# Kernel tuning notes

Hardware: AMD Instinct MI355X
Metric: run time of the kernel (lower is better)

## Reference

```python
import jax, jax.numpy as jnp
import numpy as np

B, IN, H = 4096, 1024, 1024
G = 5  # i, f, o, c_hat, s gates

def setup_inputs() -> dict:
    key = jax.random.key(0)
    ks = jax.random.split(key, 24)
    s_in = 1.0 / np.sqrt(IN)
    s_h = 1.0 / np.sqrt(H)
    s_cat = 1.0 / np.sqrt(IN + H)
    inp = {
        'x': jax.random.normal(ks[0], (B, IN), jnp.float32),
        'h_prev': jax.random.normal(ks[1], (B, H), jnp.float32),
        'c_prev': jax.random.normal(ks[2], (B, H), jnp.float32),
        'ssg_state': jax.random.normal(ks[3], (B, H), jnp.float32),
        # stacked gate weights, torch Linear convention y = x @ W.T + b
        'Wx': jax.random.uniform(ks[4], (G, H, IN), jnp.float32, -s_in, s_in),
        'bWx': jax.random.uniform(ks[5], (G, H), jnp.float32, -s_in, s_in),
        'Ux': jax.random.uniform(ks[6], (G, H, H), jnp.float32, -s_h, s_h),
        'bUx': jax.random.uniform(ks[7], (G, H), jnp.float32, -s_h, s_h),
        # alpha MLP: Linear(IN+H -> H), ReLU, Linear(H -> 1), Sigmoid
        'a1_w': jax.random.uniform(ks[8], (H, IN + H), jnp.float32, -s_cat, s_cat),
        'a1_b': jax.random.uniform(ks[9], (H,), jnp.float32, -s_cat, s_cat),
        'a2_w': jax.random.uniform(ks[10], (1, H), jnp.float32, -s_h, s_h),
        'a2_b': jax.random.uniform(ks[11], (1,), jnp.float32, -s_h, s_h),
        'r1_w': jax.random.uniform(ks[12], (H, H), jnp.float32, -s_h, s_h),
        'r1_b': jax.random.uniform(ks[13], (H,), jnp.float32, -s_h, s_h),
        'r2_w': jax.random.uniform(ks[14], (H, H), jnp.float32, -s_h, s_h),
        'r2_b': jax.random.uniform(ks[15], (H,), jnp.float32, -s_h, s_h),
        'r3_w': jax.random.uniform(ks[16], (H, H), jnp.float32, -s_h, s_h),
        'r3_b': jax.random.uniform(ks[17], (H,), jnp.float32, -s_h, s_h),
        'ssg_w': jax.random.uniform(ks[18], (H, H), jnp.float32, -s_h, s_h),
        'ssg_b': jax.random.uniform(ks[19], (H,), jnp.float32, -s_h, s_h),
    }
    return inp


def reference(x, h_prev, c_prev, ssg_state, Wx, bWx, Ux, bUx,
              a1_w, a1_b, a2_w, a2_b, r1_w, r1_b, r2_w, r2_b, r3_w, r3_b,
              ssg_w, ssg_b):
    # all 5 gate pre-activations in two batched GEMMs: [G, B, H]
    g = (jnp.einsum('bi,ghi->gbh', x, Wx) + bWx[:, None, :]
         + jnp.einsum('bh,gkh->gbk', h_prev, Ux) + bUx[:, None, :])
    i_t = jax.nn.sigmoid(g[0])
    f_t = jax.nn.sigmoid(g[1])
    o_t = jax.nn.sigmoid(g[2])
    c_hat_t = jnp.tanh(g[3])
    s_t = jax.nn.sigmoid(g[4])  # computed as in original (unused when ssg_state given)

    combined = jnp.concatenate([x, h_prev], axis=-1)  # [B, IN+H]
    a_hidden = jax.nn.relu(combined @ a1_w.T + a1_b)
    alpha_t = jax.nn.sigmoid(a_hidden @ a2_w.T + a2_b)  # [B, 1]

    ssg_new = (ssg_state + h_prev) @ ssg_w.T + ssg_b  # ssg_state is not None branch

    c_t = f_t * c_prev + i_t * c_hat_t * s_t * alpha_t * ssg_new

    r = jax.nn.relu(h_prev @ r1_w.T + r1_b)
    r = jax.nn.relu(r @ r2_w.T + r2_b)
    residual = r @ r3_w.T + r3_b

    c_t = c_t + residual
    h_t = o_t * jnp.tanh(c_t)
    return (h_t, c_t, ssg_new)
```

## Files before the change

### kernel.cpp

```cpp
#include <hip/hip_runtime.h>
#include <hip/hip_bf16.h>

#define B_DIM 4096
#define H_DIM 1024
#define K1    2048
#define N1    6144
#define N2    2048
#define NT1   (K1 / 64)

typedef __attribute__((ext_vector_type(8))) short bf16x8;
typedef __attribute__((ext_vector_type(4))) float f32x4;

__device__ __forceinline__ unsigned short f2bf(float f) {
  unsigned int x = __float_as_uint(f);
  x += 0x7fffu + ((x >> 16) & 1u);
  return (unsigned short)(x >> 16);
}
__device__ __forceinline__ float bf2f(unsigned short u) {
  return __uint_as_float(((unsigned int)u) << 16);
}
__device__ __forceinline__ float fast_sigmoid(float x) {
  return __builtin_amdgcn_rcpf(1.0f + __expf(-x));
}
__device__ __forceinline__ float fast_tanh(float x) {
  return 1.0f - 2.0f * __builtin_amdgcn_rcpf(1.0f + __expf(2.0f * x));
}
__device__ __forceinline__ void gload_lds16(const void* g, void* l) {
  __builtin_amdgcn_global_load_lds(
      (const __attribute__((address_space(1))) void*)g,
      (__attribute__((address_space(3))) void*)l, 16, 0, 0);
}

__device__ __forceinline__ int swz1k(int x) {
  return x ^ (((x >> 9) & 1) << 5);
}

__global__ __launch_bounds__(256) void prep_kernel(
    const float* __restrict__ x, const float* __restrict__ h,
    const float* __restrict__ ssg_state,
    const float* __restrict__ Wx, const float* __restrict__ Ux,
    const float* __restrict__ a1_w,
    const float* __restrict__ ssg_w, const float* __restrict__ r1_w,
    const float* __restrict__ r2_w, const float* __restrict__ r3_w,
    unsigned short* __restrict__ combined,
    unsigned short* __restrict__ ssg_in,
    unsigned short* __restrict__ hprev_bf,
    unsigned short* __restrict__ W1,
    unsigned short* __restrict__ W2,
    unsigned short* __restrict__ W3,
    unsigned short* __restrict__ W4)
{
  const size_t NV0 = (size_t)B_DIM * K1 / 4;
  const size_t NV1 = (size_t)B_DIM * H_DIM / 4;
  const size_t NV2 = NV1;
  const size_t NV3 = (size_t)N1 * K1 / 4;
  const size_t NV4 = (size_t)N2 * H_DIM / 4;
  const size_t NV5 = (size_t)H_DIM * H_DIM / 4;
  const size_t total = NV0 + NV1 + NV2 + NV3 + NV4 + NV5 + NV5;
  const size_t stride = (size_t)gridDim.x * blockDim.x;

  for (size_t v = (size_t)blockIdx.x * blockDim.x + threadIdx.x; v < total; v += stride) {
    size_t idx = v;
    const float* src;
    unsigned short* dst;
    if (idx < NV0) {
      size_t e = idx * 4, b = e >> 11, k = e & 2047;
      src = (k < 1024) ? &x[(b << 10) + k] : &h[(b << 10) + (k - 1024)];
      dst = &combined[e];
    } else if ((idx -= NV0) < NV1) {
      size_t e = idx * 4;
      float4 a = *(const float4*)&ssg_state[e];
      float4 c = *(const float4*)&h[e];
      ushort4 o;
      o.x = f2bf(a.x + c.x); o.y = f2bf(a.y + c.y);
      o.z = f2bf(a.z + c.z); o.w = f2bf(a.w + c.w);
      *(ushort4*)&ssg_in[e] = o;
      continue;
    } else if ((idx -= NV1) < NV2) {
      size_t e = idx * 4; src = &h[e]; dst = &hprev_bf[e];
    } else if ((idx -= NV2) < NV3) {
      size_t e = idx * 4, n = e >> 11, k = e & 2047;
      if (n < 5120) src = (k < 1024) ? &Wx[(n << 10) + k] : &Ux[(n << 10) + (k - 1024)];
      else          src = &a1_w[((n - 5120) << 11) + k];
      dst = &W1[e];
    } else if ((idx -= NV3) < NV4) {
      size_t e = idx * 4, n = e >> 10, k = e & 1023;
      src = (n < 1024) ? &ssg_w[(n << 10) + k] : &r1_w[((n - 1024) << 10) + k];
      dst = &W2[e];
    } else if ((idx -= NV4) < NV5) {
      size_t e = idx * 4; src = &r2_w[e]; dst = &W3[e];
    } else {
      idx -= NV5;
      size_t e = idx * 4; src = &r3_w[e]; dst = &W4[e];
    }
    float4 a = *(const float4*)src;
    ushort4 o;
    o.x = f2bf(a.x); o.y = f2bf(a.y); o.z = f2bf(a.z); o.w = f2bf(a.w);
    *(ushort4*)dst = o;
  }
}

__global__ __launch_bounds__(512, 2) void gemm8p_mode0(
    const unsigned short* __restrict__ A,
    const unsigned short* __restrict__ W,
    const float* __restrict__ bWx, const float* __restrict__ bUx,
    const float* __restrict__ a1_b,
    unsigned short* __restrict__ gates,
    unsigned short* __restrict__ a_hidden)
{
  __shared__ unsigned short lds[49152];

  const int tid  = threadIdx.x;
  const int wave = tid >> 6;
  const int lane = tid & 63;
  const int wm = wave >> 2;
  const int wn = wave & 3;

  const int NWG = (B_DIM / 128) * (N1 / 256);
  const int swz = (blockIdx.x & 7) * (NWG / 8) + (blockIdx.x >> 3);
  const int ntn = N1 / 256;
  const int tm = swz / ntn, tn = swz % ntn;
  const int tmB = tm * 128, tnB = tn * 256;

  const int sidx = swz1k(lane * 16);
  const int r_l  = sidx >> 6;
  const int kel  = (sidx & 63) >> 1;
  const unsigned short* pA[2];
  const unsigned short* pB[2];
#pragma unroll
  for (int j = 0; j < 2; ++j) {
    const int rr = wave * 16 + r_l;
    const int kk0 = j * 32 + kel;
    pA[j] = A + (size_t)(tmB + rr) * K1 + kk0;
    pB[j] = W + (size_t)(tnB + rr) * K1 + kk0;
  }

#define STAGE_A(tt) do { const int p_ = (tt) & 1;                                \
    gload_lds16(pA[0] + (size_t)(tt) * 64,                                       \
                &lds[p_ * 24576 + (wave * 2 + 0) * 512]);                        \
    gload_lds16(pA[1] + (size_t)(tt) * 64,                                       \
                &lds[p_ * 24576 + (wave * 2 + 1) * 512]); } while (0)
#define STAGE_B(tt, h_) do { const int p_ = (tt) & 1;                            \
    gload_lds16(pB[0] + (size_t)(h_) * 128 * K1 + (tt) * 64,                     \
                &lds[p_ * 24576 + 8192 + (h_) * 8192 + (wave * 2 + 0) * 512]);   \
    gload_lds16(pB[1] + (size_t)(h_) * 128 * K1 + (tt) * 64,                     \
                &lds[p_ * 24576 + 8192 + (h_) * 8192 + (wave * 2 + 1) * 512]); } while (0)

  const int loc = swz1k((lane & 15) * 64 + (lane >> 4) * 16);

  f32x4 acc[4][4];
#pragma unroll
  for (int m = 0; m < 4; ++m)
#pragma unroll
    for (int n = 0; n < 4; ++n) acc[m][n] = (f32x4){0.f, 0.f, 0.f, 0.f};

  STAGE_A(0); STAGE_B(0, 0); STAGE_B(0, 1);

#define MFMA16(aV, bV) do {                                                      \
    _Pragma("unroll")                                                            \
    for (int n = 0; n < 4; ++n) {                                                \
      _Pragma("unroll")                                                          \
      for (int m = 0; m < 4; ++m)                                                \
        acc[m][n] = __builtin_amdgcn_mfma_f32_16x16x32_bf16(                     \
            aV[m], bV[n], acc[m][n], 0, 0, 0);                                   \
    } } while (0)

  const char* lchar = (const char*)lds;
  for (int t = 0; t < NT1; ++t) {
    asm volatile("s_waitcnt vmcnt(0)" ::: "memory");
    __builtin_amdgcn_s_barrier();

    const char* base = lchar + (t & 1) * 49152;
    const char* bA = base + wm * 8192 + loc;
    const char* bB = base + 16384 + wn * 8192 + loc;

    bf16x8 a0[4], a1[4], b0[4], b1[4];
#pragma unroll
    for (int n = 0; n < 4; ++n) b0[n] = *(const bf16x8*)(bB + (2 * n + 0) * 1024);
#pragma unroll
    for (int m = 0; m < 4; ++m) a0[m] = *(const bf16x8*)(bA + (2 * m + 0) * 1024);
    if (t + 1 < NT1) STAGE_A(t + 1);
#pragma unroll
    for (int n = 0; n < 4; ++n) b1[n] = *(const bf16x8*)(bB + (2 * n + 1) * 1024);
#pragma unroll
    for (int m = 0; m < 4; ++m) a1[m] = *(const bf16x8*)(bA + (2 * m + 1) * 1024);
    if (t + 1 < NT1) { STAGE_B(t + 1, 0); STAGE_B(t + 1, 1); }

    __builtin_amdgcn_s_setprio(1);
    MFMA16(a0, b0);
    __builtin_amdgcn_s_setprio(0);
    __builtin_amdgcn_s_setprio(1);
    MFMA16(a1, b1);
    __builtin_amdgcn_s_setprio(0);
  }
#undef MFMA16
#undef STAGE_A
#undef STAGE_B

  unsigned short* slab = &lds[wave * 1024];
  const int l15 = lane & 15, lq4 = (lane >> 4) << 2;
  const int lr8 = lane >> 3, lc8 = lane & 7;
  const bool isgate = (tn < 20);
  const int g = tn >> 2;
  const int colg0 = (isgate ? (tn & 3) : (tn - 20)) * 256 + wn * 64;
  unsigned short* outbase = isgate ? (gates + (size_t)g * ((size_t)B_DIM * 1024))
                                   : a_hidden;
  const int rowg0 = tmB + wm * 64;
  float biasv[4];
#pragma unroll
  for (int fn = 0; fn < 4; ++fn) {
    const int c = colg0 + fn * 16 + l15;
    biasv[fn] = isgate ? (bWx[g * 1024 + c] + bUx[g * 1024 + c]) : a1_b[c];
  }
  __builtin_amdgcn_s_barrier();
#pragma unroll
  for (int fm = 0; fm < 4; ++fm) {
#pragma unroll
    for (int fn = 0; fn < 4; ++fn) {
      f32x4 v = acc[fm][fn];
#pragma unroll
      for (int j = 0; j < 4; ++j) {
        const int row = lq4 + j;
        const float xv = v[j] + biasv[fn];
        const float res = isgate ? ((g == 3) ? fast_tanh(xv) : fast_sigmoid(xv))
                                 : fmaxf(xv, 0.f);
        const int colb = ((fn * 16 + l15) * 2) ^ (((row >> 2) & 3) << 5);
        slab[(row * 128 + colb) >> 1] = f2bf(res);
      }
    }
    asm volatile("s_waitcnt lgkmcnt(0)" ::: "memory");
    __builtin_amdgcn_sched_barrier(0);
#pragma unroll
    for (int rd = 0; rd < 2; ++rd) {
      const int row = rd * 8 + lr8;
      const int cb = (lc8 * 16) ^ (((row >> 2) & 3) << 5);
      bf16x8 pk = *(const bf16x8*)((const char*)slab + row * 128 + cb);
      const size_t r = (size_t)(rowg0 + fm * 16 + row);
      *(bf16x8*)&outbase[r * 1024 + colg0 + lc8 * 8] = pk;
    }
    asm volatile("s_waitcnt lgkmcnt(0)" ::: "memory");
    __builtin_amdgcn_sched_barrier(0);
  }
}

template <int MODE>
__global__ __launch_bounds__(256, 3) void gemm_bf16(
    const unsigned short* __restrict__ A0g,
    const unsigned short* __restrict__ A1g,
    const unsigned short* __restrict__ Wg,
    const int M, const int N, const int K,
    const float* __restrict__ b0, const float* __restrict__ b1,
    void* __restrict__ out0, void* __restrict__ out1)
{
  __shared__ unsigned short As[128 * 64];
  __shared__ unsigned short Bs[128 * 64];

  const int tid  = threadIdx.x;
  const int wave = tid >> 6;
  const int lane = tid & 63;
  const int wm = wave >> 1, wn = wave & 1;

  const int ntn = N >> 7;
  const int tm = blockIdx.x / ntn;
  const int tn = blockIdx.x % ntn;

  const unsigned short* Ag = A0g;
  if (MODE == 1 && tn >= 8) Ag = A1g;

  const int lrow = lane >> 3;
  const int lk   = (lane & 7) * 8;
  size_t a_off[4], b_off[4];
#pragma unroll
  for (int i = 0; i < 4; ++i) {
    int c = wave * 4 + i;
    int row = c * 8 + lrow;
    a_off[i] = (size_t)(tm * 128 + row) * K + lk;
    b_off[i] = (size_t)(tn * 128 + row) * K + lk;
  }

  f32x4 acc[4][4];
#pragma unroll
  for (int m = 0; m < 4; ++m)
#pragma unroll
    for (int n = 0; n < 4; ++n) acc[m][n] = (f32x4){0.f, 0.f, 0.f, 0.f};

  const int arow  = wm * 64 + (lane & 15);
  const int brow  = wn * 64 + (lane & 15);
  const int kfrag = (lane >> 4) * 8;

  for (int k0 = 0; k0 < K; k0 += 64) {
#pragma unroll
    for (int i = 0; i < 4; ++i) {
      gload_lds16(Ag + a_off[i] + k0, &As[(wave * 4 + i) * 512]);
      gload_lds16(Wg + b_off[i] + k0, &Bs[(wave * 4 + i) * 512]);
    }
    __syncthreads();
#pragma unroll
    for (int kk = 0; kk < 2; ++kk) {
      bf16x8 af[4], bfr[4];
#pragma unroll
      for (int m = 0; m < 4; ++m)
        af[m] = *(const bf16x8*)&As[(arow + m * 16) * 64 + kk * 32 + kfrag];
#pragma unroll
      for (int n = 0; n < 4; ++n)
        bfr[n] = *(const bf16x8*)&Bs[(brow + n * 16) * 64 + kk * 32 + kfrag];
#pragma unroll
      for (int m = 0; m < 4; ++m)
#pragma unroll
        for (int n = 0; n < 4; ++n)
          acc[m][n] = __builtin_amdgcn_mfma_f32_16x16x32_bf16(
              af[m], bfr[n], acc[m][n], 0, 0, 0);
    }
    __syncthreads();
  }

  const int col0 = tn * 128 + wn * 64;
  const int row0 = tm * 128 + wm * 64 + ((lane >> 4) << 2);
#pragma unroll
  for (int n = 0; n < 4; ++n) {
    const int col = col0 + n * 16 + (lane & 15);
    float bias;
    if (MODE == 1)      bias = (col < 1024) ? b0[col] : b1[col - 1024];
    else                bias = b0[col];
#pragma unroll
    for (int m = 0; m < 4; ++m) {
      const int rowb = row0 + m * 16;
      f32x4 v = acc[m][n];
#pragma unroll
      for (int j = 0; j < 4; ++j) {
        const float xv = v[j] + bias;
        const int r = rowb + j;
        if (MODE == 1) {
          if (col < 1024) {
            ((float*)out0)[(size_t)r * 1024 + col] = xv;
          } else {
            ((unsigned short*)out1)[(size_t)r * 1024 + (col - 1024)] = f2bf(fmaxf(xv, 0.f));
          }
        } else if (MODE == 2) {
          ((unsigned short*)out0)[(size_t)r * 1024 + col] = f2bf(fmaxf(xv, 0.f));
        } else {
          ((float*)out0)[(size_t)r * 1024 + col] = xv;
        }
      }
    }
  }
}

__global__ __launch_bounds__(256) void alpha_kernel(
    const unsigned short* __restrict__ a_hidden,
    const float* __restrict__ a2_w, const float* __restrict__ a2_b,
    float* __restrict__ alpha)
{
  const int wave = threadIdx.x >> 6, lane = threadIdx.x & 63;
  const int row = blockIdx.x * 4 + wave;
  const unsigned short* ah = a_hidden + (size_t)row * 1024;
  float sum = 0.f;
#pragma unroll
  for (int half = 0; half < 2; ++half) {
    const int h0 = half * 512 + lane * 8;
    ushort4 u0 = *(const ushort4*)&ah[h0];
    ushort4 u1 = *(const ushort4*)&ah[h0 + 4];
    float4 w0 = *(const float4*)&a2_w[h0];
    float4 w1 = *(const float4*)&a2_w[h0 + 4];
    sum += bf2f(u0.x) * w0.x + bf2f(u0.y) * w0.y + bf2f(u0.z) * w0.z + bf2f(u0.w) * w0.w;
    sum += bf2f(u1.x) * w1.x + bf2f(u1.y) * w1.y + bf2f(u1.z) * w1.z + bf2f(u1.w) * w1.w;
  }
#pragma unroll
  for (int off = 32; off; off >>= 1) sum += __shfl_xor(sum, off);
  if (lane == 0) alpha[row] = fast_sigmoid(sum + a2_b[0]);
}

__global__ __launch_bounds__(256) void final_elem_kernel(
    const unsigned short* __restrict__ gates,
    const float* __restrict__ c_prev,
    const float* __restrict__ alpha,
    const float* __restrict__ residual,
    const float* __restrict__ ssg_new,
    float* __restrict__ h_out, float* __restrict__ c_out)
{
  const size_t BH = (size_t)B_DIM * H_DIM;
  const size_t e = ((size_t)blockIdx.x * blockDim.x + threadIdx.x) * 4;
  if (e >= BH) return;
  const float al = alpha[e >> 10];
  ushort4 iu = *(const ushort4*)&gates[e];
  ushort4 fu = *(const ushort4*)&gates[BH + e];
  ushort4 ou = *(const ushort4*)&gates[2 * BH + e];
  ushort4 cu = *(const ushort4*)&gates[3 * BH + e];
  ushort4 su = *(const ushort4*)&gates[4 * BH + e];
  float4 cp = *(const float4*)&c_prev[e];
  float4 rs = *(const float4*)&residual[e];
  float4 sg = *(const float4*)&ssg_new[e];
  float4 ho, co;
  co.x = bf2f(fu.x) * cp.x + bf2f(iu.x) * bf2f(cu.x) * bf2f(su.x) * al * sg.x + rs.x;
  co.y = bf2f(fu.y) * cp.y + bf2f(iu.y) * bf2f(cu.y) * bf2f(su.y) * al * sg.y + rs.y;
  co.z = bf2f(fu.z) * cp.z + bf2f(iu.z) * bf2f(cu.z) * bf2f(su.z) * al * sg.z + rs.z;
  co.w = bf2f(fu.w) * cp.w + bf2f(iu.w) * bf2f(cu.w) * bf2f(su.w) * al * sg.w + rs.w;
  ho.x = bf2f(ou.x) * fast_tanh(co.x);
  ho.y = bf2f(ou.y) * fast_tanh(co.y);
  ho.z = bf2f(ou.z) * fast_tanh(co.z);
  ho.w = bf2f(ou.w) * fast_tanh(co.w);
  *(float4*)&h_out[e] = ho;
  *(float4*)&c_out[e] = co;
}

extern "C" void kernel_launch(void* const* d_in, const int* in_sizes, int n_in,
                              void* d_out, int out_size, void* d_ws, size_t ws_size,
                              hipStream_t stream)
{
  (void)in_sizes; (void)n_in; (void)out_size; (void)ws_size;
  const float* x         = (const float*)d_in[0];
  const float* h_prev    = (const float*)d_in[1];
  const float* c_prev    = (const float*)d_in[2];
  const float* ssg_state = (const float*)d_in[3];
  const float* Wx        = (const float*)d_in[4];
  const float* bWx       = (const float*)d_in[5];
  const float* Ux        = (const float*)d_in[6];
  const float* bUx       = (const float*)d_in[7];
  const float* a1_w      = (const float*)d_in[8];
  const float* a1_b      = (const float*)d_in[9];
  const float* a2_w      = (const float*)d_in[10];
  const float* a2_b      = (const float*)d_in[11];
  const float* r1_w      = (const float*)d_in[12];
  const float* r1_b      = (const float*)d_in[13];
  const float* r2_w      = (const float*)d_in[14];
  const float* r2_b      = (const float*)d_in[15];
  const float* r3_w      = (const float*)d_in[16];
  const float* r3_b      = (const float*)d_in[17];
  const float* ssg_w     = (const float*)d_in[18];
  const float* ssg_b     = (const float*)d_in[19];

  char* ws = (char*)d_ws;
  unsigned short* combined = (unsigned short*)(ws);
  unsigned short* ssg_in   = (unsigned short*)(ws + 16777216);
  unsigned short* hprev_bf = (unsigned short*)(ws + 25165824);
  unsigned short* W1       = (unsigned short*)(ws + 33554432);
  unsigned short* W2       = (unsigned short*)(ws + 58720256);
  unsigned short* W3       = (unsigned short*)(ws + 62914560);
  unsigned short* W4       = (unsigned short*)(ws + 65011712);
  unsigned short* gates    = (unsigned short*)(ws + 67108864);
  unsigned short* a_hidden = (unsigned short*)(ws + 109051904);
  float*          alpha    = (float*)(ws + 117440512);
  unsigned short* r1       = (unsigned short*)(ws + 117456896);
  unsigned short* r2       = (unsigned short*)(ws + 125845504);
  float*          residual = (float*)(ws + 134234112);

  float* h_out   = (float*)d_out;
  float* c_out   = h_out + (size_t)B_DIM * H_DIM;
  float* ssg_out = c_out + (size_t)B_DIM * H_DIM;

  prep_kernel<<<4096, 256, 0, stream>>>(x, h_prev, ssg_state, Wx, Ux, a1_w,
                                        ssg_w, r1_w, r2_w, r3_w,
                                        combined, ssg_in, hprev_bf, W1, W2, W3, W4);

  gemm8p_mode0<<<(B_DIM / 128) * (N1 / 256), 512, 0, stream>>>(
      combined, W1, bWx, bUx, a1_b, gates, a_hidden);

  gemm_bf16<1><<<(B_DIM / 128) * (N2 / 128), 256, 0, stream>>>(
      ssg_in, hprev_bf, W2, B_DIM, N2, 1024, ssg_b, r1_b, ssg_out, r1);

  gemm_bf16<2><<<(B_DIM / 128) * (1024 / 128), 256, 0, stream>>>(
      r1, r1, W3, B_DIM, 1024, 1024, r2_b, nullptr, r2, nullptr);

  gemm_bf16<3><<<(B_DIM / 128) * (1024 / 128), 256, 0, stream>>>(
      r2, r2, W4, B_DIM, 1024, 1024, r3_b, nullptr, residual, nullptr);

  alpha_kernel<<<B_DIM / 4, 256, 0, stream>>>(a_hidden, a2_w, a2_b, alpha);

  final_elem_kernel<<<(B_DIM * H_DIM / 4) / 256, 256, 0, stream>>>(
      gates, c_prev, alpha, residual, ssg_out, h_out, c_out);
}
```

Before: 269.8 us.

## Add pipelined 128x256 GEMM for ssg/r1, reuse combined h, fuse alpha into final

Replaces the generic 128x128 GEMM for the ssg/r1 stage with a 512-thread 128x256-tile kernel. The new kernel uses double-buffered LDS with swizzled direct-to-LDS loads, a block-index swizzle, and an LDS-staged bf16 store for r1. It reads h_prev directly from the bf16 combined buffer with a 2048 stride, so the prep kernel no longer writes a separate hprev_bf copy. The alpha MLP reduction is folded into the final elementwise kernel, one block per row, which removes a launch and the alpha buffer. The larger tile raises LDS and register use and may lower occupancy.

```diff
diff --git a/kernel.cpp b/kernel.cpp
--- a/kernel.cpp
+++ b/kernel.cpp
@@ -5,8 +5,8 @@
 #define H_DIM 1024
 #define K1    2048
 #define N1    6144
-#define N2    2048
 #define NT1   (K1 / 64)
+#define NT2   16
 
 typedef __attribute__((ext_vector_type(8))) short bf16x8;
 typedef __attribute__((ext_vector_type(4))) float f32x4;
@@ -44,7 +44,6 @@
     const float* __restrict__ r2_w, const float* __restrict__ r3_w,
     unsigned short* __restrict__ combined,
     unsigned short* __restrict__ ssg_in,
-    unsigned short* __restrict__ hprev_bf,
     unsigned short* __restrict__ W1,
     unsigned short* __restrict__ W2,
     unsigned short* __restrict__ W3,
@@ -52,11 +51,10 @@
 {
   const size_t NV0 = (size_t)B_DIM * K1 / 4;
   const size_t NV1 = (size_t)B_DIM * H_DIM / 4;
-  const size_t NV2 = NV1;
   const size_t NV3 = (size_t)N1 * K1 / 4;
-  const size_t NV4 = (size_t)N2 * H_DIM / 4;
+  const size_t NV4 = (size_t)2048 * H_DIM / 4;
   const size_t NV5 = (size_t)H_DIM * H_DIM / 4;
-  const size_t total = NV0 + NV1 + NV2 + NV3 + NV4 + NV5 + NV5;
+  const size_t total = NV0 + NV1 + NV3 + NV4 + NV5 + NV5;
   const size_t stride = (size_t)gridDim.x * blockDim.x;
 
   for (size_t v = (size_t)blockIdx.x * blockDim.x + threadIdx.x; v < total; v += stride) {
@@ -76,9 +74,7 @@
       o.z = f2bf(a.z + c.z); o.w = f2bf(a.w + c.w);
       *(ushort4*)&ssg_in[e] = o;
       continue;
-    } else if ((idx -= NV1) < NV2) {
-      size_t e = idx * 4; src = &h[e]; dst = &hprev_bf[e];
-    } else if ((idx -= NV2) < NV3) {
+    } else if ((idx -= NV1) < NV3) {
       size_t e = idx * 4, n = e >> 11, k = e & 2047;
       if (n < 5120) src = (k < 1024) ? &Wx[(n << 10) + k] : &Ux[(n << 10) + (k - 1024)];
       else          src = &a1_w[((n - 5120) << 11) + k];
@@ -243,14 +239,166 @@
   }
 }
 
+__global__ __launch_bounds__(512, 2) void gemm_n2048(
+    const unsigned short* __restrict__ A0,
+    const unsigned short* __restrict__ A1,
+    const unsigned short* __restrict__ W,
+    const float* __restrict__ ssg_b, const float* __restrict__ r1_b,
+    float* __restrict__ ssg_out,
+    unsigned short* __restrict__ r1)
+{
+  __shared__ unsigned short lds[49152];
+
+  const int tid  = threadIdx.x;
+  const int wave = tid >> 6;
+  const int lane = tid & 63;
+  const int wm = wave >> 2;
+  const int wn = wave & 3;
+
+  const int swz = (blockIdx.x & 7) * 32 + (blockIdx.x >> 3);
+  const int tm = swz >> 3, tn = swz & 7;
+  const int tmB = tm * 128, tnB = tn * 256;
+
+  const unsigned short* Abase = (tn < 4) ? A0 : A1;
+  const int lda = (tn < 4) ? 1024 : 2048;
+
+  const int sidx = swz1k(lane * 16);
+  const int r_l  = sidx >> 6;
+  const int kel  = (sidx & 63) >> 1;
+  const unsigned short* pA[2];
+  const unsigned short* pB[2];
+#pragma unroll
+  for (int j = 0; j < 2; ++j) {
+    const int rr = wave * 16 + r_l;
+    const int kk0 = j * 32 + kel;
+    pA[j] = Abase + (size_t)(tmB + rr) * lda + kk0;
+    pB[j] = W + (size_t)(tnB + rr) * 1024 + kk0;
+  }
+
+#define STAGE_A(tt) do { const int p_ = (tt) & 1;                                \
+    gload_lds16(pA[0] + (size_t)(tt) * 64,                                       \
+                &lds[p_ * 24576 + (wave * 2 + 0) * 512]);                        \
+    gload_lds16(pA[1] + (size_t)(tt) * 64,                                       \
+                &lds[p_ * 24576 + (wave * 2 + 1) * 512]); } while (0)
+#define STAGE_B(tt, h_) do { const int p_ = (tt) & 1;                            \
+    gload_lds16(pB[0] + (size_t)(h_) * 128 * 1024 + (tt) * 64,                   \
+                &lds[p_ * 24576 + 8192 + (h_) * 8192 + (wave * 2 + 0) * 512]);   \
+    gload_lds16(pB[1] + (size_t)(h_) * 128 * 1024 + (tt) * 64,                   \
+                &lds[p_ * 24576 + 8192 + (h_) * 8192 + (wave * 2 + 1) * 512]); } while (0)
+
+  const int loc = swz1k((lane & 15) * 64 + (lane >> 4) * 16);
+
+  f32x4 acc[4][4];
+#pragma unroll
+  for (int m = 0; m < 4; ++m)
+#pragma unroll
+    for (int n = 0; n < 4; ++n) acc[m][n] = (f32x4){0.f, 0.f, 0.f, 0.f};
+
+  STAGE_A(0); STAGE_B(0, 0); STAGE_B(0, 1);
+
+#define MFMA16(aV, bV) do {                                                      \
+    _Pragma("unroll")                                                            \
+    for (int n = 0; n < 4; ++n) {                                                \
+      _Pragma("unroll")                                                          \
+      for (int m = 0; m < 4; ++m)                                                \
+        acc[m][n] = __builtin_amdgcn_mfma_f32_16x16x32_bf16(                     \
+            aV[m], bV[n], acc[m][n], 0, 0, 0);                                   \
+    } } while (0)
+
+  const char* lchar = (const char*)lds;
+  for (int t = 0; t < NT2; ++t) {
+    asm volatile("s_waitcnt vmcnt(0)" ::: "memory");
+    __builtin_amdgcn_s_barrier();
+
+    const char* base = lchar + (t & 1) * 49152;
+    const char* bA = base + wm * 8192 + loc;
+    const char* bB = base + 16384 + wn * 8192 + loc;
+
+    bf16x8 a0[4], a1[4], b0[4], b1[4];
+#pragma unroll
+    for (int n = 0; n < 4; ++n) b0[n] = *(const bf16x8*)(bB + (2 * n + 0) * 1024);
+#pragma unroll
+    for (int m = 0; m < 4; ++m) a0[m] = *(const bf16x8*)(bA + (2 * m + 0) * 1024);
+    if (t + 1 < NT2) STAGE_A(t + 1);
+#pragma unroll
+    for (int n = 0; n < 4; ++n) b1[n] = *(const bf16x8*)(bB + (2 * n + 1) * 1024);
+#pragma unroll
+    for (int m = 0; m < 4; ++m) a1[m] = *(const bf16x8*)(bA + (2 * m + 1) * 1024);
+    if (t + 1 < NT2) { STAGE_B(t + 1, 0); STAGE_B(t + 1, 1); }
+
+    __builtin_amdgcn_s_setprio(1);
+    MFMA16(a0, b0);
+    __builtin_amdgcn_s_setprio(0);
+    __builtin_amdgcn_s_setprio(1);
+    MFMA16(a1, b1);
+    __builtin_amdgcn_s_setprio(0);
+  }
+#undef MFMA16
+#undef STAGE_A
+#undef STAGE_B
+
+  const int l15 = lane & 15, lq4 = (lane >> 4) << 2;
+  const int rowg0 = tmB + wm * 64;
+  if (tn < 4) {
+    const int col0 = tn * 256 + wn * 64;
+#pragma unroll
+    for (int fn = 0; fn < 4; ++fn) {
+      const int col = col0 + fn * 16 + l15;
+      const float bias = ssg_b[col];
+#pragma unroll
+      for (int fm = 0; fm < 4; ++fm) {
+        f32x4 v = acc[fm][fn];
+#pragma unroll
+        for (int j = 0; j < 4; ++j) {
+          const int r = rowg0 + fm * 16 + lq4 + j;
+          ssg_out[(size_t)r * 1024 + col] = v[j] + bias;
+        }
+      }
+    }
+  } else {
+    unsigned short* slab = &lds[wave * 1024];
+    const int lr8 = lane >> 3, lc8 = lane & 7;
+    const int colg0 = (tn - 4) * 256 + wn * 64;
+    float biasv[4];
+#pragma unroll
+    for (int fn = 0; fn < 4; ++fn) biasv[fn] = r1_b[colg0 + fn * 16 + l15];
+    __builtin_amdgcn_s_barrier();
+#pragma unroll
+    for (int fm = 0; fm < 4; ++fm) {
+#pragma unroll
+      for (int fn = 0; fn < 4; ++fn) {
+        f32x4 v = acc[fm][fn];
+#pragma unroll
+        for (int j = 0; j < 4; ++j) {
+          const int row = lq4 + j;
+          const float res = fmaxf(v[j] + biasv[fn], 0.f);
+          const int colb = ((fn * 16 + l15) * 2) ^ (((row >> 2) & 3) << 5);
+          slab[(row * 128 + colb) >> 1] = f2bf(res);
+        }
+      }
+      asm volatile("s_waitcnt lgkmcnt(0)" ::: "memory");
+      __builtin_amdgcn_sched_barrier(0);
+#pragma unroll
+      for (int rd = 0; rd < 2; ++rd) {
+        const int row = rd * 8 + lr8;
+        const int cb = (lc8 * 16) ^ (((row >> 2) & 3) << 5);
+        bf16x8 pk = *(const bf16x8*)((const char*)slab + row * 128 + cb);
+        const size_t r = (size_t)(rowg0 + fm * 16 + row);
+        *(bf16x8*)&r1[r * 1024 + colg0 + lc8 * 8] = pk;
+      }
+      asm volatile("s_waitcnt lgkmcnt(0)" ::: "memory");
+      __builtin_amdgcn_sched_barrier(0);
+    }
+  }
+}
+
 template <int MODE>
 __global__ __launch_bounds__(256, 3) void gemm_bf16(
     const unsigned short* __restrict__ A0g,
-    const unsigned short* __restrict__ A1g,
     const unsigned short* __restrict__ Wg,
     const int M, const int N, const int K,
-    const float* __restrict__ b0, const float* __restrict__ b1,
-    void* __restrict__ out0, void* __restrict__ out1)
+    const float* __restrict__ b0,
+    void* __restrict__ out0)
 {
   __shared__ unsigned short As[128 * 64];
   __shared__ unsigned short Bs[128 * 64];
@@ -263,9 +411,6 @@
   const int ntn = N >> 7;
   const int tm = blockIdx.x / ntn;
   const int tn = blockIdx.x % ntn;
-
-  const unsigned short* Ag = A0g;
-  if (MODE == 1 && tn >= 8) Ag = A1g;
 
   const int lrow = lane >> 3;
   const int lk   = (lane & 7) * 8;
@@ -291,7 +436,7 @@
   for (int k0 = 0; k0 < K; k0 += 64) {
 #pragma unroll
     for (int i = 0; i < 4; ++i) {
-      gload_lds16(Ag + a_off[i] + k0, &As[(wave * 4 + i) * 512]);
+      gload_lds16(A0g + a_off[i] + k0, &As[(wave * 4 + i) * 512]);
       gload_lds16(Wg + b_off[i] + k0, &Bs[(wave * 4 + i) * 512]);
     }
     __syncthreads();
@@ -319,9 +464,7 @@
 #pragma unroll
   for (int n = 0; n < 4; ++n) {
     const int col = col0 + n * 16 + (lane & 15);
-    float bias;
-    if (MODE == 1)      bias = (col < 1024) ? b0[col] : b1[col - 1024];
-    else                bias = b0[col];
+    const float bias = b0[col];
 #pragma unroll
     for (int m = 0; m < 4; ++m) {
       const int rowb = row0 + m * 16;
@@ -330,13 +473,7 @@
       for (int j = 0; j < 4; ++j) {
         const float xv = v[j] + bias;
         const int r = rowb + j;
-        if (MODE == 1) {
-          if (col < 1024) {
-            ((float*)out0)[(size_t)r * 1024 + col] = xv;
-          } else {
-            ((unsigned short*)out1)[(size_t)r * 1024 + (col - 1024)] = f2bf(fmaxf(xv, 0.f));
-          }
-        } else if (MODE == 2) {
+        if (MODE == 2) {
           ((unsigned short*)out0)[(size_t)r * 1024 + col] = f2bf(fmaxf(xv, 0.f));
         } else {
           ((float*)out0)[(size_t)r * 1024 + col] = xv;
@@ -346,42 +483,35 @@
   }
 }
 
-__global__ __launch_bounds__(256) void alpha_kernel(
+__global__ __launch_bounds__(256) void final_fused(
+    const unsigned short* __restrict__ gates,
+    const float* __restrict__ c_prev,
     const unsigned short* __restrict__ a_hidden,
     const float* __restrict__ a2_w, const float* __restrict__ a2_b,
-    float* __restrict__ alpha)
-{
-  const int wave = threadIdx.x >> 6, lane = threadIdx.x & 63;
-  const int row = blockIdx.x * 4 + wave;
-  const unsigned short* ah = a_hidden + (size_t)row * 1024;
-  float sum = 0.f;
-#pragma unroll
-  for (int half = 0; half < 2; ++half) {
-    const int h0 = half * 512 + lane * 8;
-    ushort4 u0 = *(const ushort4*)&ah[h0];
-    ushort4 u1 = *(const ushort4*)&ah[h0 + 4];
-    float4 w0 = *(const float4*)&a2_w[h0];
-    float4 w1 = *(const float4*)&a2_w[h0 + 4];
-    sum += bf2f(u0.x) * w0.x + bf2f(u0.y) * w0.y + bf2f(u0.z) * w0.z + bf2f(u0.w) * w0.w;
-    sum += bf2f(u1.x) * w1.x + bf2f(u1.y) * w1.y + bf2f(u1.z) * w1.z + bf2f(u1.w) * w1.w;
-  }
-#pragma unroll
-  for (int off = 32; off; off >>= 1) sum += __shfl_xor(sum, off);
-  if (lane == 0) alpha[row] = fast_sigmoid(sum + a2_b[0]);
-}
-
-__global__ __launch_bounds__(256) void final_elem_kernel(
-    const unsigned short* __restrict__ gates,
-    const float* __restrict__ c_prev,
-    const float* __restrict__ alpha,
     const float* __restrict__ residual,
     const float* __restrict__ ssg_new,
     float* __restrict__ h_out, float* __restrict__ c_out)
 {
+  __shared__ float red[5];
+  const int r = blockIdx.x;
+  const int tid = threadIdx.x;
   const size_t BH = (size_t)B_DIM * H_DIM;
-  const size_t e = ((size_t)blockIdx.x * blockDim.x + threadIdx.x) * 4;
-  if (e >= BH) return;
-  const float al = alpha[e >> 10];
+
+  {
+    ushort4 u = *(const ushort4*)&a_hidden[(size_t)r * 1024 + tid * 4];
+    float4 w = *(const float4*)&a2_w[tid * 4];
+    float s = bf2f(u.x) * w.x + bf2f(u.y) * w.y + bf2f(u.z) * w.z + bf2f(u.w) * w.w;
+#pragma unroll
+    for (int off = 32; off; off >>= 1) s += __shfl_xor(s, off);
+    if ((tid & 63) == 0) red[tid >> 6] = s;
+  }
+  __syncthreads();
+  if (tid == 0)
+    red[4] = fast_sigmoid(red[0] + red[1] + red[2] + red[3] + a2_b[0]);
+  __syncthreads();
+  const float al = red[4];
+
+  const size_t e = (size_t)r * 1024 + tid * 4;
   ushort4 iu = *(const ushort4*)&gates[e];
   ushort4 fu = *(const ushort4*)&gates[BH + e];
   ushort4 ou = *(const ushort4*)&gates[2 * BH + e];
@@ -432,14 +562,12 @@
   char* ws = (char*)d_ws;
   unsigned short* combined = (unsigned short*)(ws);
   unsigned short* ssg_in   = (unsigned short*)(ws + 16777216);
-  unsigned short* hprev_bf = (unsigned short*)(ws + 25165824);
   unsigned short* W1       = (unsigned short*)(ws + 33554432);
   unsigned short* W2       = (unsigned short*)(ws + 58720256);
   unsigned short* W3       = (unsigned short*)(ws + 62914560);
   unsigned short* W4       = (unsigned short*)(ws + 65011712);
   unsigned short* gates    = (unsigned short*)(ws + 67108864);
   unsigned short* a_hidden = (unsigned short*)(ws + 109051904);
-  float*          alpha    = (float*)(ws + 117440512);
   unsigned short* r1       = (unsigned short*)(ws + 117456896);
   unsigned short* r2       = (unsigned short*)(ws + 125845504);
   float*          residual = (float*)(ws + 134234112);
@@ -450,22 +578,20 @@
 
   prep_kernel<<<4096, 256, 0, stream>>>(x, h_prev, ssg_state, Wx, Ux, a1_w,
                                         ssg_w, r1_w, r2_w, r3_w,
-                                        combined, ssg_in, hprev_bf, W1, W2, W3, W4);
+                                        combined, ssg_in, W1, W2, W3, W4);
 
   gemm8p_mode0<<<(B_DIM / 128) * (N1 / 256), 512, 0, stream>>>(
       combined, W1, bWx, bUx, a1_b, gates, a_hidden);
 
-  gemm_bf16<1><<<(B_DIM / 128) * (N2 / 128), 256, 0, stream>>>(
-      ssg_in, hprev_bf, W2, B_DIM, N2, 1024, ssg_b, r1_b, ssg_out, r1);
+  gemm_n2048<<<256, 512, 0, stream>>>(
+      ssg_in, combined + 1024, W2, ssg_b, r1_b, ssg_out, r1);
 
   gemm_bf16<2><<<(B_DIM / 128) * (1024 / 128), 256, 0, stream>>>(
-      r1, r1, W3, B_DIM, 1024, 1024, r2_b, nullptr, r2, nullptr);
+      r1, W3, B_DIM, 1024, 1024, r2_b, r2);
 
   gemm_bf16<3><<<(B_DIM / 128) * (1024 / 128), 256, 0, stream>>>(
-      r2, r2, W4, B_DIM, 1024, 1024, r3_b, nullptr, residual, nullptr);
-
-  alpha_kernel<<<B_DIM / 4, 256, 0, stream>>>(a_hidden, a2_w, a2_b, alpha);
-
-  final_elem_kernel<<<(B_DIM * H_DIM / 4) / 256, 256, 0, stream>>>(
-      gates, c_prev, alpha, residual, ssg_out, h_out, c_out);
-}
+      r2, W4, B_DIM, 1024, 1024, r3_b, residual);
+
+  final_fused<<<B_DIM, 256, 0, stream>>>(
+      gates, c_prev, a_hidden, a2_w, a2_b, residual, ssg_out, h_out, c_out);
+}
```

Result: faster. 254.2 us (-5.8%).
